# Kernel tuning notes

Measured on AMD Instinct MI355X. Metric: run time of the kernel, lower is better.

The kernel has to match this reference:

```python
import jax, jax.numpy as jnp
import numpy as np

N_NODES = 40000
N_EDGES = 640000
IN_CH = 128
HID = 128
OUT_CH = 16
N_GRAPHS = 64
EPS = 1e-16


def segment_softmax(logits, seg, num_segments):
    m = jax.ops.segment_max(logits, seg, num_segments=num_segments)
    e = jnp.exp(logits - m[seg])
    s = jax.ops.segment_sum(e, seg, num_segments=num_segments)
    return e / (s[seg] + EPS)


def gt_conv(x, src, dst, W, b, att):
    # x: [N, Cin] -> h: [N, C]
    h = x @ W + b
    s = h @ att  # [N] per-node attention score (att broadcast over rows)
    # alpha_e = <x_i, att> + <x_j, att>; x_i = target (dst), x_j = source (src)
    alpha = s[dst] + s[src]
    alpha = jax.nn.leaky_relu(alpha, negative_slope=0.2)
    # PyG code normalizes over edge_index[0] groups (source nodes)
    alpha = segment_softmax(alpha, src, x.shape[0])
    msg = h[src] * alpha[:, None]
    return jax.ops.segment_sum(msg, dst, num_segments=x.shape[0])


def gcn_conv(x, src, dst, W, b):
    n = x.shape[0]
    h = x @ W
    deg = jax.ops.segment_sum(jnp.ones_like(src, dtype=h.dtype), dst, num_segments=n)
    dinv = jnp.where(deg > 0, deg ** -0.5, 0.0)
    norm = dinv[src] * dinv[dst]
    out = jax.ops.segment_sum(h[src] * norm[:, None], dst, num_segments=n)
    return out + b


def setup_inputs() -> dict:
    key = jax.random.key(0)
    ks = jax.random.split(key, 12)
    x = jax.random.normal(ks[0], (N_NODES, IN_CH), dtype=jnp.float32)
    edge_index = jax.random.randint(ks[1], (2, N_EDGES), 0, N_NODES, dtype=jnp.int32)
    batch = jnp.sort(jax.random.randint(ks[2], (N_NODES,), 0, N_GRAPHS, dtype=jnp.int32))
    def glorot(k, shape):
        fan_in, fan_out = shape[0], shape[-1]
        lim = jnp.sqrt(6.0 / (fan_in + fan_out))
        return jax.random.uniform(k, shape, jnp.float32, -lim, lim)
    return {
        "x": x, "edge_index": edge_index, "batch": batch,
        "W1": glorot(ks[3], (IN_CH, HID)), "b1": jnp.zeros((HID,), jnp.float32),
        "att1": glorot(ks[4], (1, HID))[0],
        "W2": glorot(ks[5], (HID, HID)), "b2": jnp.zeros((HID,), jnp.float32),
        "att2": glorot(ks[6], (1, HID))[0],
        "Wg": glorot(ks[7], (HID, HID)), "bg": jnp.zeros((HID,), jnp.float32),
        "Wfc": glorot(ks[8], (HID, OUT_CH)), "bfc": jnp.zeros((OUT_CH,), jnp.float32),
    }


def reference(x, edge_index, batch, W1, b1, att1, W2, b2, att2, Wg, bg, Wfc, bfc):
    n = x.shape[0]
    loops = jnp.arange(n, dtype=edge_index.dtype)
    src = jnp.concatenate([edge_index[0], loops])
    dst = jnp.concatenate([edge_index[1], loops])
    # two GT layers (dropout is identity in eval mode)
    h = jax.nn.relu(gt_conv(x, src, dst, W1, b1, att1))
    h = jax.nn.relu(gt_conv(h, src, dst, W2, b2, att2))
    # GCNConv (with self loops, symmetric normalization)
    h = gcn_conv(h, src, dst, Wg, bg)
    # global mean pool over graphs
    sums = jax.ops.segment_sum(h, batch, num_segments=N_GRAPHS)
    counts = jax.ops.segment_sum(jnp.ones((n,), h.dtype), batch, num_segments=N_GRAPHS)
    pooled = sums / jnp.maximum(counts, 1.0)[:, None]
    logits = pooled @ Wfc + bfc
    return jax.nn.log_softmax(logits, axis=1)
```

## Files before the change

### kernel.cpp

```cpp
#include <hip/hip_runtime.h>
#include <hip/hip_fp16.h>
#include <hip/hip_fp8.h>
#include <math.h>

#define NN 40000
#define NE 640000
#define ET 680000
#define CH 128
#define OC 16
#define NG 64
#define NQ (ET/4)
#define CAP 48
#define NFILLB 665
#define NGEMMB 625
#define NBLK1 (2*NGEMMB + (NFILLB - NGEMMB))

typedef _Float16 h8 __attribute__((ext_vector_type(8)));
typedef float    f4 __attribute__((ext_vector_type(4)));

__device__ __forceinline__ float2 fp8x2_to_f32(unsigned short v) {
    __hip_fp8_e4m3 a, b;
    a.__x = (__hip_fp8_storage_t)(v & 0xff);
    b.__x = (__hip_fp8_storage_t)(v >> 8);
    return make_float2((float)a, (float)b);
}
__device__ __forceinline__ unsigned char f32_to_fp8(float f) {
    __hip_fp8_e4m3 t(f);
    return (unsigned char)t.__x;
}

__global__ __launch_bounds__(256)
void prep(const int* __restrict__ batch, int* __restrict__ gstart,
          int* __restrict__ cur_d, int* __restrict__ cur_s,
          float* __restrict__ pooled,
          const float* __restrict__ W1, const float* __restrict__ W2,
          const float* __restrict__ Wg, _Float16* __restrict__ Wt1,
          _Float16* __restrict__ Wt2, _Float16* __restrict__ Wtg)
{
    int i = blockIdx.x * 256 + threadIdx.x;
    if (i < NN) {
        cur_d[i] = 0; cur_s[i] = 0;
        int b = batch[i];
        if (i == 0) { for (int g = 0; g <= b; ++g) gstart[g] = 0; }
        else { int pb = batch[i - 1]; for (int g = pb + 1; g <= b; ++g) gstart[g] = i; }
        if (i == NN - 1) { for (int g = b + 1; g <= NG; ++g) gstart[g] = NN; }
    }
    if (i < NG * CH) pooled[i] = 0.f;
    if (i < CH * CH) {
        int k = i >> 7, n = i & 127;
        Wt1[n * CH + k] = (_Float16)W1[i];
        Wt2[n * CH + k] = (_Float16)W2[i];
        Wtg[n * CH + k] = (_Float16)Wg[i];
    }
}

__device__ __forceinline__
void stage_w(_Float16 (*wt)[136], const _Float16* __restrict__ Wt, int tid)
{
#pragma unroll
    for (int i = 0; i < 8; ++i) {
        int f = tid + i * 256;
        int n = f >> 4, c8 = f & 15;
        *(float4*)&wt[n][c8 * 8] = *(const float4*)(Wt + (size_t)n * CH + c8 * 8);
    }
}

template<bool BIAS, bool ATTN>
__device__ __forceinline__
void mfma_body(_Float16 (*xs)[136], _Float16 (*wt)[136],
               const float* __restrict__ bias, const float* __restrict__ att,
               unsigned char* __restrict__ out8, float* __restrict__ s,
               int rb, int tid)
{
    const int wv = tid >> 6, lane = tid & 63;
    const int m = lane & 15, quad = lane >> 4;
    f4 acc[8] = {};
#pragma unroll
    for (int ks = 0; ks < 4; ++ks) {
        h8 a = *(const h8*)&xs[wv * 16 + m][ks * 32 + quad * 8];
#pragma unroll
        for (int t = 0; t < 8; ++t) {
            h8 b = *(const h8*)&wt[t * 16 + m][ks * 32 + quad * 8];
            acc[t] = __builtin_amdgcn_mfma_f32_16x16x32_f16(a, b, acc[t], 0, 0, 0);
        }
    }
    float pr[4] = {0.f, 0.f, 0.f, 0.f};
#pragma unroll
    for (int t = 0; t < 8; ++t) {
        int col = t * 16 + m;
        float bv = BIAS ? bias[col] : 0.f;
        float av = ATTN ? att[col] : 0.f;
#pragma unroll
        for (int r = 0; r < 4; ++r) {
            float o = acc[t][r] + bv;
            int row = rb + wv * 16 + quad * 4 + r;
            out8[(size_t)row * CH + col] = f32_to_fp8(o);
            if (ATTN) pr[r] += o * av;
        }
    }
    if (ATTN) {
#pragma unroll
        for (int r = 0; r < 4; ++r) {
            float p = pr[r];
            p += __shfl_xor(p, 1); p += __shfl_xor(p, 2);
            p += __shfl_xor(p, 4); p += __shfl_xor(p, 8);
            if (m == 0) s[rb + wv * 16 + quad * 4 + r] = p;
        }
    }
}

__device__ __forceinline__
void fill_body(int fb, int tid, const int* __restrict__ ei,
               int* __restrict__ cur_d, int* __restrict__ cur_s,
               unsigned short* __restrict__ pad_src,
               unsigned short* __restrict__ pad_dst)
{
    int q = fb * 256 + tid;
    if (q >= NQ) return;
    int e0 = q * 4;
    int4 sv, dv;
    if (e0 < NE) {
        sv = *(const int4*)(ei + e0);
        dv = *(const int4*)(ei + NE + e0);
    } else {
        int b = e0 - NE;
        sv = make_int4(b, b + 1, b + 2, b + 3);
        dv = sv;
    }
    const int* sc = (const int*)&sv;
    const int* dc = (const int*)&dv;
#pragma unroll
    for (int u = 0; u < 4; ++u) {
        int srcE = sc[u], dstE = dc[u];
        int p = atomicAdd(cur_d + dstE, 1);
        if (p < CAP) pad_src[dstE * CAP + p] = (unsigned short)srcE;
        int p2 = atomicAdd(cur_s + srcE, 1);
        if (p2 < CAP) pad_dst[srcE * CAP + p2] = (unsigned short)dstE;
    }
}

__global__ __launch_bounds__(256)
void fill_gemm1(const float* __restrict__ x, const _Float16* __restrict__ Wt1,
                const float* __restrict__ b1, const float* __restrict__ att1,
                unsigned char* __restrict__ out8, float* __restrict__ s1,
                const int* __restrict__ ei, int* __restrict__ cur_d,
                int* __restrict__ cur_s, unsigned short* __restrict__ pad_src,
                unsigned short* __restrict__ pad_dst)
{
    __shared__ __attribute__((aligned(16))) _Float16 xs[64][136];
    __shared__ __attribute__((aligned(16))) _Float16 wt[128][136];
    int bid = blockIdx.x;
    if (bid < 2 * NGEMMB && (bid & 1) == 0) {
        int g = bid >> 1;
        int rb = g * 64, tid = threadIdx.x;
#pragma unroll
        for (int i = 0; i < 4; ++i) {
            int f = tid + i * 256;
            int r = f >> 4, c8 = f & 15;
            const float* p = x + (size_t)(rb + r) * CH + c8 * 8;
            float4 v0 = *(const float4*)p;
            float4 v1 = *(const float4*)(p + 4);
            __half2 h[4] = { __floats2half2_rn(v0.x, v0.y), __floats2half2_rn(v0.z, v0.w),
                             __floats2half2_rn(v1.x, v1.y), __floats2half2_rn(v1.z, v1.w) };
            *(float4*)&xs[r][c8 * 8] = *(float4*)h;
        }
        stage_w(wt, Wt1, tid);
        __syncthreads();
        mfma_body<true, true>(xs, wt, b1, att1, out8, s1, rb, tid);
        return;
    }
    int fb = (bid < 2 * NGEMMB) ? (bid >> 1) : (NGEMMB + (bid - 2 * NGEMMB));
    if (fb < NFILLB)
        fill_body(fb, threadIdx.x, ei, cur_d, cur_s, pad_src, pad_dst);
}

template<bool RELU, bool BIAS, bool ATTN>
__global__ __launch_bounds__(256)
void gemm_k(const __half* __restrict__ in, const _Float16* __restrict__ Wt,
            const float* __restrict__ bias, const float* __restrict__ att,
            unsigned char* __restrict__ out8, float* __restrict__ s)
{
    __shared__ __attribute__((aligned(16))) _Float16 xs[64][136];
    __shared__ __attribute__((aligned(16))) _Float16 wt[128][136];
    const int tid = threadIdx.x;
    const int rb = blockIdx.x * 64;
#pragma unroll
    for (int i = 0; i < 4; ++i) {
        int f = tid + i * 256;
        int r = f >> 4, c8 = f & 15;
        float4 raw = *(const float4*)(in + (size_t)(rb + r) * CH + c8 * 8);
        if (RELU) {
            __half2* h2 = (__half2*)&raw;
#pragma unroll
            for (int u = 0; u < 4; ++u) {
                float2 fv = __half22float2(h2[u]);
                h2[u] = __floats2half2_rn(fmaxf(fv.x, 0.f), fmaxf(fv.y, 0.f));
            }
        }
        *(float4*)&xs[r][c8 * 8] = raw;
    }
    stage_w(wt, Wt, tid);
    __syncthreads();
    mfma_body<BIAS, ATTN>(xs, wt, bias, att, out8, s, rb, tid);
}

__global__ __launch_bounds__(256)
void softmax_stats(const int* __restrict__ cur_s,
                   const unsigned short* __restrict__ pad_dst,
                   const float* __restrict__ s, float* __restrict__ ssum)
{
    int node = (blockIdx.x * 256 + threadIdx.x) >> 6;
    int lane = threadIdx.x & 63;
    if (node >= NN) return;
    int deg = min(cur_s[node], CAP);
    float si = s[node];
    float sum = 0.f;
    if (lane < deg) {
        int d = pad_dst[node * CAP + lane];
        float t = si + s[d];
        t = t > 0.f ? t : 0.2f * t;
        sum = expf(t);
    }
#pragma unroll
    for (int o = 32; o; o >>= 1) sum += __shfl_xor(sum, o);
    if (lane == 0) ssum[node] = sum;
}

__device__ __forceinline__
void gather_core(int node, int lane, int deg, int src, float w,
                 const unsigned char* __restrict__ h8p, __half* __restrict__ out16)
{
    int qtr = lane >> 4, cl = lane & 15;
    float a[8] = {};
    for (int base = 0; base < deg; base += 8) {
        uint2 v[2]; float wj[2];
#pragma unroll
        for (int u = 0; u < 2; ++u) {
            int e = base + 4 * u + qtr;
            int sj = __shfl(src, e);
            wj[u]  = __shfl(w, e);
            v[u] = ((const uint2*)(h8p + (size_t)sj * CH))[cl];
        }
#pragma unroll
        for (int u = 0; u < 2; ++u) {
            float2 p0 = fp8x2_to_f32((unsigned short)(v[u].x & 0xffff));
            float2 p1 = fp8x2_to_f32((unsigned short)(v[u].x >> 16));
            float2 p2 = fp8x2_to_f32((unsigned short)(v[u].y & 0xffff));
            float2 p3 = fp8x2_to_f32((unsigned short)(v[u].y >> 16));
            a[0] += p0.x * wj[u]; a[1] += p0.y * wj[u];
            a[2] += p1.x * wj[u]; a[3] += p1.y * wj[u];
            a[4] += p2.x * wj[u]; a[5] += p2.y * wj[u];
            a[6] += p3.x * wj[u]; a[7] += p3.y * wj[u];
        }
    }
#pragma unroll
    for (int k = 0; k < 8; ++k) {
        a[k] += __shfl_xor(a[k], 16);
        a[k] += __shfl_xor(a[k], 32);
    }
    if (qtr == 0) {
        float4 st;
        ((__half2*)&st)[0] = __floats2half2_rn(a[0], a[1]);
        ((__half2*)&st)[1] = __floats2half2_rn(a[2], a[3]);
        ((__half2*)&st)[2] = __floats2half2_rn(a[4], a[5]);
        ((__half2*)&st)[3] = __floats2half2_rn(a[6], a[7]);
        ((float4*)(out16 + (size_t)node * CH))[cl] = st;
    }
}

__global__ __launch_bounds__(256)
void gt_gather(const int* __restrict__ cur_d,
               const unsigned short* __restrict__ pad_src,
               const unsigned char* __restrict__ h8p, const float* __restrict__ s,
               const float* __restrict__ ssum, __half* __restrict__ out16)
{
    int node = (blockIdx.x * 256 + threadIdx.x) >> 6;
    int lane = threadIdx.x & 63;
    if (node >= NN) return;
    int deg = min(cur_d[node], CAP);
    float sd = s[node];
    int src = 0; float w = 0.f;
    if (lane < deg) {
        src = pad_src[node * CAP + lane];
        float t = sd + s[src];
        t = t > 0.f ? t : 0.2f * t;
        w = expf(t) / ssum[src];
    }
    gather_core(node, lane, deg, src, w, h8p, out16);
}

__global__ __launch_bounds__(256)
void gcn_gather(const int* __restrict__ cur_d,
                const unsigned short* __restrict__ pad_src,
                const unsigned char* __restrict__ h8p, __half* __restrict__ out16)
{
    int node = (blockIdx.x * 256 + threadIdx.x) >> 6;
    int lane = threadIdx.x & 63;
    if (node >= NN) return;
    int dn = cur_d[node];
    int deg = min(dn, CAP);
    float nu = rsqrtf((float)max(dn, 1));
    int src = 0; float w = 0.f;
    if (lane < deg) {
        src = pad_src[node * CAP + lane];
        w = rsqrtf((float)max(cur_d[src], 1)) * nu;
    }
    gather_core(node, lane, deg, src, w, h8p, out16);
}

__global__ __launch_bounds__(128)
void pool_part(const __half* __restrict__ h16, const int* __restrict__ batch,
               float* __restrict__ pooled)
{
    int ch = threadIdx.x;
    int start = blockIdx.x * 80;
    float acc = 0.f;
    int curg = batch[start];
    for (int base = start; base < start + 80; base += 8) {
        float vals[8]; int gs[8];
#pragma unroll
        for (int u = 0; u < 8; ++u)
            vals[u] = __half2float(h16[(size_t)(base + u) * CH + ch]);
#pragma unroll
        for (int u = 0; u < 8; ++u) gs[u] = batch[base + u];
#pragma unroll
        for (int u = 0; u < 8; ++u) {
            if (gs[u] != curg) {
                atomicAdd(pooled + (size_t)curg * CH + ch, acc);
                acc = 0.f; curg = gs[u];
            }
            acc += vals[u];
        }
    }
    atomicAdd(pooled + (size_t)curg * CH + ch, acc);
}

__global__ __launch_bounds__(256)
void head_kernel(const float* __restrict__ psum, const int* __restrict__ gstart,
                 const float* __restrict__ bg, const float* __restrict__ Wfc,
                 const float* __restrict__ bfc, float* __restrict__ out)
{
    __shared__ float lg[NG][OC];
    int tid = threadIdx.x;
#pragma unroll
    for (int i = 0; i < 4; ++i) {
        int f = tid + i * 256;
        int g = f >> 4, o = f & 15;
        float cnt = fmaxf((float)(gstart[g + 1] - gstart[g]), 1.0f);
        float inv = 1.0f / cnt;
        float acc = bfc[o];
        for (int c = 0; c < CH; ++c)
            acc += (psum[g * CH + c] * inv + bg[c]) * Wfc[c * OC + o];
        lg[g][o] = acc;
    }
    __syncthreads();
    if (tid < NG) {
        float m = -1e30f;
#pragma unroll
        for (int o = 0; o < OC; ++o) m = fmaxf(m, lg[tid][o]);
        float sum = 0.f;
#pragma unroll
        for (int o = 0; o < OC; ++o) sum += expf(lg[tid][o] - m);
        float lse = m + logf(sum);
#pragma unroll
        for (int o = 0; o < OC; ++o) out[tid * OC + o] = lg[tid][o] - lse;
    }
}

extern "C" void kernel_launch(void* const* d_in, const int* in_sizes, int n_in,
                              void* d_out, int out_size, void* d_ws, size_t ws_size,
                              hipStream_t stream)
{
    const float* x     = (const float*)d_in[0];
    const int*   ei    = (const int*)d_in[1];
    const int*   batch = (const int*)d_in[2];
    const float* W1    = (const float*)d_in[3];
    const float* b1    = (const float*)d_in[4];
    const float* att1  = (const float*)d_in[5];
    const float* W2    = (const float*)d_in[6];
    const float* b2    = (const float*)d_in[7];
    const float* att2  = (const float*)d_in[8];
    const float* Wg    = (const float*)d_in[9];
    const float* bg    = (const float*)d_in[10];
    const float* Wfc   = (const float*)d_in[11];
    const float* bfc   = (const float*)d_in[12];
    float* out = (float*)d_out;

    const size_t NNCH = (size_t)NN * CH;
    __half* B16 = (__half*)d_ws;
    unsigned char* A8 = (unsigned char*)(B16 + NNCH);
    _Float16* Wt1 = (_Float16*)(A8 + NNCH);
    _Float16* Wt2 = Wt1 + CH * CH;
    _Float16* Wtg = Wt2 + CH * CH;
    int*   cur_d  = (int*)(Wtg + CH * CH);
    int*   cur_s  = cur_d + NN;
    float* s1     = (float*)(cur_s + NN);
    float* s2     = s1 + NN;
    float* pooled = s2 + NN;
    float* ssum   = pooled + NG * CH;
    int*   gstart = (int*)(ssum + NN);
    unsigned short* pad_src = (unsigned short*)(gstart + NG + 1);
    unsigned short* pad_dst = pad_src + (size_t)NN * CAP;

    const int WB = NN / 4;

    prep<<<157, 256, 0, stream>>>(batch, gstart, cur_d, cur_s, pooled,
                                  W1, W2, Wg, Wt1, Wt2, Wtg);

    fill_gemm1<<<NBLK1, 256, 0, stream>>>(
        x, Wt1, b1, att1, A8, s1, ei, cur_d, cur_s, pad_src, pad_dst);
    softmax_stats<<<WB, 256, 0, stream>>>(cur_s, pad_dst, s1, ssum);
    gt_gather<<<WB, 256, 0, stream>>>(cur_d, pad_src, A8, s1, ssum, B16);

    gemm_k<true, true, true><<<NGEMMB, 256, 0, stream>>>(
        B16, Wt2, b2, att2, A8, s2);
    softmax_stats<<<WB, 256, 0, stream>>>(cur_s, pad_dst, s2, ssum);
    gt_gather<<<WB, 256, 0, stream>>>(cur_d, pad_src, A8, s2, ssum, B16);

    gemm_k<true, false, false><<<NGEMMB, 256, 0, stream>>>(
        B16, Wtg, nullptr, nullptr, A8, nullptr);
    gcn_gather<<<WB, 256, 0, stream>>>(cur_d, pad_src, A8, B16);

    pool_part<<<500, 128, 0, stream>>>(B16, batch, pooled);
    head_kernel<<<1, 256, 0, stream>>>(pooled, gstart, bg, Wfc, bfc, out);
}
```

Baseline: 273.0 us.

## Fold GCN weight into head by reassociating aggregation and pooling, drop GCN GEMM

Since the GCN layer is linear, aggregation and mean pooling commute with the Wg projection. The change applies the GCN aggregation directly to the layer-2 output and fuses Wg@Wfc and the bias into a small precomputed 128x16 matrix used in the head. This removes the whole third GEMM launch. The layer-2 gather now writes fp8 (with ReLU applied) as the GCN gather input, and the gcn output is split across reused buffers. The cost is extra fp8 quantisation of activations before aggregation, which may shift accuracy.

```diff
diff --git a/kernel.cpp b/kernel.cpp
--- a/kernel.cpp
+++ b/kernel.cpp
@@ -14,6 +14,7 @@
 #define NFILLB 665
 #define NGEMMB 625
 #define NBLK1 (2*NGEMMB + (NFILLB - NGEMMB))
+#define NSPLIT 20000
 
 typedef _Float16 h8 __attribute__((ext_vector_type(8)));
 typedef float    f4 __attribute__((ext_vector_type(4)));
@@ -34,8 +35,10 @@
           int* __restrict__ cur_d, int* __restrict__ cur_s,
           float* __restrict__ pooled,
           const float* __restrict__ W1, const float* __restrict__ W2,
-          const float* __restrict__ Wg, _Float16* __restrict__ Wt1,
-          _Float16* __restrict__ Wt2, _Float16* __restrict__ Wtg)
+          const float* __restrict__ Wg, const float* __restrict__ Wfc,
+          const float* __restrict__ bg, const float* __restrict__ bfc,
+          _Float16* __restrict__ Wt1, _Float16* __restrict__ Wt2,
+          float* __restrict__ Wgf, float* __restrict__ bgf)
 {
     int i = blockIdx.x * 256 + threadIdx.x;
     if (i < NN) {
@@ -50,7 +53,20 @@
         int k = i >> 7, n = i & 127;
         Wt1[n * CH + k] = (_Float16)W1[i];
         Wt2[n * CH + k] = (_Float16)W2[i];
-        Wtg[n * CH + k] = (_Float16)Wg[i];
+    }
+    if (i < CH * OC) {
+        int k = i >> 4, o = i & 15;
+        float acc = 0.f;
+        for (int c = 0; c < CH; ++c)
+            acc += Wg[k * CH + c] * Wfc[c * OC + o];
+        Wgf[k * OC + o] = acc;
+    }
+    if (i >= CH * OC && i < CH * OC + OC) {
+        int o = i - CH * OC;
+        float acc = bfc[o];
+        for (int c = 0; c < CH; ++c)
+            acc += bg[c] * Wfc[c * OC + o];
+        bgf[o] = acc;
     }
 }
 
@@ -226,9 +242,10 @@
     if (lane == 0) ssum[node] = sum;
 }
 
+template<int OM>
 __device__ __forceinline__
 void gather_core(int node, int lane, int deg, int src, float w,
-                 const unsigned char* __restrict__ h8p, __half* __restrict__ out16)
+                 const unsigned char* __restrict__ h8p, void* __restrict__ outrow)
 {
     int qtr = lane >> 4, cl = lane & 15;
     float a[8] = {};
@@ -259,20 +276,34 @@
         a[k] += __shfl_xor(a[k], 32);
     }
     if (qtr == 0) {
-        float4 st;
-        ((__half2*)&st)[0] = __floats2half2_rn(a[0], a[1]);
-        ((__half2*)&st)[1] = __floats2half2_rn(a[2], a[3]);
-        ((__half2*)&st)[2] = __floats2half2_rn(a[4], a[5]);
-        ((__half2*)&st)[3] = __floats2half2_rn(a[6], a[7]);
-        ((float4*)(out16 + (size_t)node * CH))[cl] = st;
-    }
-}
-
+        if (OM == 0) {
+            float4 st;
+            ((__half2*)&st)[0] = __floats2half2_rn(a[0], a[1]);
+            ((__half2*)&st)[1] = __floats2half2_rn(a[2], a[3]);
+            ((__half2*)&st)[2] = __floats2half2_rn(a[4], a[5]);
+            ((__half2*)&st)[3] = __floats2half2_rn(a[6], a[7]);
+            ((float4*)outrow)[cl] = st;
+        } else {
+            unsigned lo = (unsigned)f32_to_fp8(fmaxf(a[0], 0.f))
+                        | ((unsigned)f32_to_fp8(fmaxf(a[1], 0.f)) << 8)
+                        | ((unsigned)f32_to_fp8(fmaxf(a[2], 0.f)) << 16)
+                        | ((unsigned)f32_to_fp8(fmaxf(a[3], 0.f)) << 24);
+            unsigned hi = (unsigned)f32_to_fp8(fmaxf(a[4], 0.f))
+                        | ((unsigned)f32_to_fp8(fmaxf(a[5], 0.f)) << 8)
+                        | ((unsigned)f32_to_fp8(fmaxf(a[6], 0.f)) << 16)
+                        | ((unsigned)f32_to_fp8(fmaxf(a[7], 0.f)) << 24);
+            ((uint2*)outrow)[cl] = make_uint2(lo, hi);
+        }
+    }
+}
+
+template<bool F8OUT>
 __global__ __launch_bounds__(256)
 void gt_gather(const int* __restrict__ cur_d,
                const unsigned short* __restrict__ pad_src,
                const unsigned char* __restrict__ h8p, const float* __restrict__ s,
-               const float* __restrict__ ssum, __half* __restrict__ out16)
+               const float* __restrict__ ssum, __half* __restrict__ out16,
+               unsigned char* __restrict__ o8)
 {
     int node = (blockIdx.x * 256 + threadIdx.x) >> 6;
     int lane = threadIdx.x & 63;
@@ -286,13 +317,17 @@
         t = t > 0.f ? t : 0.2f * t;
         w = expf(t) / ssum[src];
     }
-    gather_core(node, lane, deg, src, w, h8p, out16);
+    if (F8OUT)
+        gather_core<1>(node, lane, deg, src, w, h8p, o8 + (size_t)node * CH);
+    else
+        gather_core<0>(node, lane, deg, src, w, h8p, out16 + (size_t)node * CH);
 }
 
 __global__ __launch_bounds__(256)
 void gcn_gather(const int* __restrict__ cur_d,
                 const unsigned short* __restrict__ pad_src,
-                const unsigned char* __restrict__ h8p, __half* __restrict__ out16)
+                const unsigned char* __restrict__ h8p,
+                __half* __restrict__ outA, __half* __restrict__ outB)
 {
     int node = (blockIdx.x * 256 + threadIdx.x) >> 6;
     int lane = threadIdx.x & 63;
@@ -305,22 +340,26 @@
         src = pad_src[node * CAP + lane];
         w = rsqrtf((float)max(cur_d[src], 1)) * nu;
     }
-    gather_core(node, lane, deg, src, w, h8p, out16);
+    __half* row = (node < NSPLIT) ? outA + (size_t)node * CH
+                                  : outB + (size_t)(node - NSPLIT) * CH;
+    gather_core<0>(node, lane, deg, src, w, h8p, row);
 }
 
 __global__ __launch_bounds__(128)
-void pool_part(const __half* __restrict__ h16, const int* __restrict__ batch,
-               float* __restrict__ pooled)
+void pool_part(const __half* __restrict__ hA, const __half* __restrict__ hB,
+               const int* __restrict__ batch, float* __restrict__ pooled)
 {
     int ch = threadIdx.x;
     int start = blockIdx.x * 80;
+    const __half* hp = (start < NSPLIT) ? hA + (size_t)start * CH
+                                        : hB + (size_t)(start - NSPLIT) * CH;
     float acc = 0.f;
     int curg = batch[start];
     for (int base = start; base < start + 80; base += 8) {
         float vals[8]; int gs[8];
 #pragma unroll
         for (int u = 0; u < 8; ++u)
-            vals[u] = __half2float(h16[(size_t)(base + u) * CH + ch]);
+            vals[u] = __half2float(hp[(size_t)(base - start + u) * CH + ch]);
 #pragma unroll
         for (int u = 0; u < 8; ++u) gs[u] = batch[base + u];
 #pragma unroll
@@ -337,8 +376,8 @@
 
 __global__ __launch_bounds__(256)
 void head_kernel(const float* __restrict__ psum, const int* __restrict__ gstart,
-                 const float* __restrict__ bg, const float* __restrict__ Wfc,
-                 const float* __restrict__ bfc, float* __restrict__ out)
+                 const float* __restrict__ Wgf, const float* __restrict__ bgf,
+                 float* __restrict__ out)
 {
     __shared__ float lg[NG][OC];
     int tid = threadIdx.x;
@@ -348,9 +387,9 @@
         int g = f >> 4, o = f & 15;
         float cnt = fmaxf((float)(gstart[g + 1] - gstart[g]), 1.0f);
         float inv = 1.0f / cnt;
-        float acc = bfc[o];
+        float acc = bgf[o];
         for (int c = 0; c < CH; ++c)
-            acc += (psum[g * CH + c] * inv + bg[c]) * Wfc[c * OC + o];
+            acc += psum[g * CH + c] * inv * Wgf[c * OC + o];
         lg[g][o] = acc;
     }
     __syncthreads();
@@ -389,38 +428,42 @@
     const size_t NNCH = (size_t)NN * CH;
     __half* B16 = (__half*)d_ws;
     unsigned char* A8 = (unsigned char*)(B16 + NNCH);
+    unsigned char* G8 = (unsigned char*)B16;
+    __half* GO_A = B16 + (size_t)NSPLIT * CH;
+    __half* GO_B = (__half*)A8;
     _Float16* Wt1 = (_Float16*)(A8 + NNCH);
     _Float16* Wt2 = Wt1 + CH * CH;
-    _Float16* Wtg = Wt2 + CH * CH;
-    int*   cur_d  = (int*)(Wtg + CH * CH);
+    float* Wgf    = (float*)(Wt2 + CH * CH);
+    float* bgf    = Wgf + CH * OC;
+    int*   cur_d  = (int*)(bgf + OC);
     int*   cur_s  = cur_d + NN;
     float* s1     = (float*)(cur_s + NN);
     float* s2     = s1 + NN;
-    float* pooled = s2 + NN;
-    float* ssum   = pooled + NG * CH;
-    int*   gstart = (int*)(ssum + NN);
+    float* ssum   = s2 + NN;
+    float* pooled = ssum + NN;
+    int*   gstart = (int*)(pooled + NG * CH);
     unsigned short* pad_src = (unsigned short*)(gstart + NG + 1);
     unsigned short* pad_dst = pad_src + (size_t)NN * CAP;
 
     const int WB = NN / 4;
 
     prep<<<157, 256, 0, stream>>>(batch, gstart, cur_d, cur_s, pooled,
-                                  W1, W2, Wg, Wt1, Wt2, Wtg);
+                                  W1, W2, Wg, Wfc, bg, bfc, Wt1, Wt2, Wgf, bgf);
 
     fill_gemm1<<<NBLK1, 256, 0, stream>>>(
         x, Wt1, b1, att1, A8, s1, ei, cur_d, cur_s, pad_src, pad_dst);
     softmax_stats<<<WB, 256, 0, stream>>>(cur_s, pad_dst, s1, ssum);
-    gt_gather<<<WB, 256, 0, stream>>>(cur_d, pad_src, A8, s1, ssum, B16);
+    gt_gather<false><<<WB, 256, 0, stream>>>(cur_d, pad_src, A8, s1, ssum,
+                                             B16, nullptr);
 
     gemm_k<true, true, true><<<NGEMMB, 256, 0, stream>>>(
         B16, Wt2, b2, att2, A8, s2);
     softmax_stats<<<WB, 256, 0, stream>>>(cur_s, pad_dst, s2, ssum);
-    gt_gather<<<WB, 256, 0, stream>>>(cur_d, pad_src, A8, s2, ssum, B16);
-
-    gemm_k<true, false, false><<<NGEMMB, 256, 0, stream>>>(
-        B16, Wtg, nullptr, nullptr, A8, nullptr);
-    gcn_gather<<<WB, 256, 0, stream>>>(cur_d, pad_src, A8, B16);
-
-    pool_part<<<500, 128, 0, stream>>>(B16, batch, pooled);
-    head_kernel<<<1, 256, 0, stream>>>(pooled, gstart, bg, Wfc, bfc, out);
-}
+    gt_gather<true><<<WB, 256, 0, stream>>>(cur_d, pad_src, A8, s2, ssum,
+                                            nullptr, G8);
+
+    gcn_gather<<<WB, 256, 0, stream>>>(cur_d, pad_src, G8, GO_A, GO_B);
+
+    pool_part<<<500, 128, 0, stream>>>(GO_A, GO_B, batch, pooled);
+    head_kernel<<<1, 256, 0, stream>>>(pooled, gstart, Wgf, bgf, out);
+}
```

New measurement: 264.7 us. 3.1% less time.
